# Kernel optimization log

Measured on AMD Instinct MI355X. Metric: run time of the kernel, lower is better.

## Reference

```python
import jax, jax.numpy as jnp
import numpy as np

N, IN_RAW, H, E, UNROLLS = 1024, 10, 96, 16384, 2

def _p(key, shape):
    return jax.random.normal(key, shape, dtype=jnp.float32) * 0.05

def setup_inputs() -> dict:
    key = jax.random.key(0)
    ks = jax.random.split(key, 24)
    x = jax.random.normal(ks[0], (N, IN_RAW), dtype=jnp.float32)
    edge_index = jax.random.randint(ks[1], (2, E), 0, N, dtype=jnp.int64)
    adj = jax.random.randint(ks[2], (N, N), 0, 2, dtype=jnp.int32)
    return {
        'x': x, 'edge_index': edge_index, 'adj': adj,
        # init_layer
        'W_init': _p(ks[3], (H, IN_RAW - 1)), 'b_init': _p(ks[4], (H,)),
        # GatedGraphConv (num_layers=1): weight [H,H], GRUCell params
        'W_ggc': _p(ks[5], (H, H)),
        'W_ih': _p(ks[6], (3 * H, H)), 'W_hh': _p(ks[7], (3 * H, H)),
        'b_ih': _p(ks[8], (3 * H,)), 'b_hh': _p(ks[9], (3 * H,)),
        # edge_attention: Linear(2H->H), Linear(H->1)
        'Wa1': _p(ks[10], (H, 2 * H)), 'ba1': _p(ks[11], (H,)),
        'Wa2': _p(ks[12], (1, H)), 'ba2': _p(ks[13], (1,)),
        # out MLP
        'Wo1': _p(ks[14], (H, H)), 'bo1': _p(ks[15], (H,)),
        'Wo2': _p(ks[16], (H, H)), 'bo2': _p(ks[17], (H,)),
        # heads
        'Wp1': _p(ks[18], (1, H)), 'bp1': _p(ks[19], (1,)),
        'Wp2': _p(ks[20], (1, H)), 'bp2': _p(ks[21], (1,)),
    }

def _leaky(v):
    return jnp.where(v >= 0, v, 0.01 * v)  # LeakyReLU default slope

def _ggnn_forward(x, edge_index, adj,
                  W_init, b_init, W_ggc, W_ih, W_hh, b_ih, b_hh,
                  Wa1, ba1, Wa2, ba2, Wo1, bo1, Wo2, bo2,
                  Wp1, bp1, Wp2, bp2):
    src, tgt = edge_index[0], edge_index[1]
    x = x[:, :-1]                                   # data.x[:, :-1]
    x = _leaky(x @ W_init.T + b_init)               # [N,H]
    adj_mask = (adj == 1)
    for _ in range(UNROLLS):
        # GatedGraphConv, 1 layer, aggr='mean'
        m = x @ W_ggc                               # [N,H]
        s = jax.ops.segment_sum(m[src], tgt, num_segments=N)
        cnt = jax.ops.segment_sum(jnp.ones((E,), x.dtype), tgt, num_segments=N)
        agg = s / jnp.maximum(cnt, 1.0)[:, None]    # mean, 0 for isolated nodes
        # GRUCell(agg, x)
        gi = agg @ W_ih.T + b_ih
        gh = x @ W_hh.T + b_hh
        ir, iz, inn = jnp.split(gi, 3, axis=1)
        hr, hz, hn = jnp.split(gh, 3, axis=1)
        r = jax.nn.sigmoid(ir + hr)
        z = jax.nn.sigmoid(iz + hz)
        n = jnp.tanh(inn + r * hn)
        x = (1.0 - z) * n + z * x
        # edge attention: concat(x_i, x_j) -> Linear(2H->H) decomposed into
        # two [H,H] halves so the NxNx2H concat tensor is never materialized.
        hi = x @ Wa1[:, :H].T                       # acts on t1 (row i)
        hj = x @ Wa1[:, H:].T                       # acts on t2 (row j)
        h = jax.nn.sigmoid(hi[:, None, :] + hj[None, :, :] + ba1)  # [N,N,H]
        coeffs = jax.nn.sigmoid(h @ Wa2[0] + ba2[0])               # [N,N]
        coeffs = jnp.where(adj_mask, coeffs, 0.0)
        x = coeffs @ x
    x = _leaky(x @ Wo1.T + bo1)
    x = _leaky(x @ Wo2.T + bo2)
    out1 = jax.nn.sigmoid(x @ Wp1.T + bp1)
    out2 = jax.nn.sigmoid(x @ Wp2.T + bp2)
    return out1, out2

def reference(x, edge_index, adj,
              W_init, b_init, W_ggc, W_ih, W_hh, b_ih, b_hh,
              Wa1, ba1, Wa2, ba2, Wo1, bo1, Wo2, bo2,
              Wp1, bp1, Wp2, bp2):
    return _ggnn_forward(x, edge_index, adj,
                         W_init, b_init, W_ggc, W_ih, W_hh, b_ih, b_hh,
                         Wa1, ba1, Wa2, ba2, Wo1, bo1, Wo2, bo2,
                         Wp1, bp1, Wp2, bp2)
```

## Files before the change

kernel.cpp:

```cpp
#include <hip/hip_runtime.h>

#define Nn 1024
#define Hh 96
#define Ee 16384
#define IN_K 9
#define IN_STRIDE 10
#define NH (Nn * Hh)
#define XS 128
#define SLOTS 64

__device__ __forceinline__ float sigf(float v) {
    return __builtin_amdgcn_rcpf(1.0f + __expf(-v));
}
__device__ __forceinline__ float tanhfast(float v) {
    float e = __expf(2.0f * v);
    return (e - 1.0f) * __builtin_amdgcn_rcpf(e + 1.0f);
}
__device__ __forceinline__ float leakyf(float v) {
    return v >= 0.0f ? v : 0.01f * v;
}

__global__ __launch_bounds__(1024) void setup_kernel(
    const float* __restrict__ W_hh, const float* __restrict__ Wa1,
    const float* __restrict__ Wo1, const float* __restrict__ Wo2,
    const float* __restrict__ W_ggc, const float* __restrict__ W_ih,
    const float* __restrict__ x_in, const float* __restrict__ W_init,
    const float* __restrict__ b_init, const int* __restrict__ ei,
    float* __restrict__ Wt_hh, float* __restrict__ Wt_a1i,
    float* __restrict__ Wt_a1j, float* __restrict__ Wt_o1,
    float* __restrict__ Wt_o2, float* __restrict__ Wf,
    float* __restrict__ xA, int* __restrict__ deg, int* __restrict__ bucket)
{
    int tid = threadIdx.x;
    int blk = blockIdx.x;
    int gt = blk * 1024 + tid;
    if (gt < 64512) {
        int idx = gt;
        if (idx < 27648) {
            int k = idx / 288, c = idx % 288;
            Wt_hh[idx] = W_hh[c * 96 + k];
        } else if ((idx -= 27648) < 9216) {
            int k = idx / 96, h2 = idx % 96;
            Wt_a1i[idx] = Wa1[h2 * 192 + k];
        } else if ((idx -= 9216) < 9216) {
            int k = idx / 96, h2 = idx % 96;
            Wt_a1j[idx] = Wa1[h2 * 192 + 96 + k];
        } else if ((idx -= 9216) < 9216) {
            int k = idx / 96, j = idx % 96;
            Wt_o1[idx] = Wo1[j * 96 + k];
        } else {
            idx -= 9216;
            int k = idx / 96, j = idx % 96;
            Wt_o2[idx] = Wo2[j * 96 + k];
        }
    }
    if (gt < 27648) {
        int k = gt / 288, c = gt % 288;
        const float* g = W_ggc + k * 96;
        const float* w = W_ih + c * 96;
        float acc = 0.0f;
        for (int j = 0; j < 96; ++j) acc += g[j] * w[j];
        Wf[gt] = acc;
    }
    if (gt < NH) {
        int n = gt / Hh, j = gt - n * Hh;
        const float* xr = x_in + n * IN_STRIDE;
        const float* wr = W_init + j * IN_K;
        float acc = b_init[j];
#pragma unroll
        for (int k = 0; k < IN_K; ++k) acc += xr[k] * wr[k];
        xA[n * XS + j] = leakyf(acc);
    }
    if (tid >= 960) {
        int e = blk * 64 + (tid - 960);
        int src = ei[e];
        int tgt = ei[Ee + e];
        int slot = atomicAdd(&deg[tgt], 1);
        if (slot < SLOTS) bucket[tgt * SLOTS + slot] = src;
    }
}

struct GShm {
    float Pg[2][4][Hh];
    float Pm[4][Hh];
    float Xr[4][Hh];
    float Xo[4][Hh];
    float gd[6][4][Hh];
    float redp[2][4][4][Hh];
};

__global__ __launch_bounds__(768) void gru_kernel(
    const float* __restrict__ xin, const int* __restrict__ deg,
    const int* __restrict__ bucket,
    const float* __restrict__ Wf, const float* __restrict__ Wt_hh,
    const float* __restrict__ b_ih, const float* __restrict__ b_hh,
    const float* __restrict__ Wt_a1i, const float* __restrict__ Wt_a1j,
    const float* __restrict__ ba1,
    float* __restrict__ xout, float* __restrict__ Ei, float* __restrict__ EjT)
{
    __shared__ GShm sh;
    int tid = threadIdx.x;
    int i0 = blockIdx.x * 4;

    {
        int h = tid % Hh;
        int rr = (tid / Hh) & 3;
        int s2 = tid / 384;
        int n = i0 + rr;
        int d = deg[n];
        int dc = d < SLOTS ? d : SLOTS;
        const int* bk = bucket + n * SLOTS;
        float acc = 0.0f;
        for (int s = s2; s < dc; s += 2)
            acc += xin[bk[s] * XS + h];
        sh.Pg[s2][rr][h] = acc;
        if (s2 == 0) sh.Xr[rr][h] = xin[n * XS + h];
    }
    __syncthreads();
    if (tid < 384) {
        int h = tid % Hh, rr = tid / Hh;
        float inv = __builtin_amdgcn_rcpf(fmaxf((float)deg[i0 + rr], 1.0f));
        sh.Pm[rr][h] = (sh.Pg[0][rr][h] + sh.Pg[1][rr][h]) * inv;
    }
    __syncthreads();

    if (tid < 576) {
        int h = tid % Hh;
        int g = tid / Hh;
        bool ipath = g < 3;
        int gc = ipath ? g : g - 3;
        const float* W = (ipath ? Wf : Wt_hh) + gc * 96 + h;
        const float (*src)[Hh] = ipath ? sh.Pm : sh.Xr;
        float a0 = 0.f, a1 = 0.f, a2 = 0.f, a3 = 0.f;
#pragma unroll 8
        for (int k = 0; k < 96; ++k) {
            float w = W[k * 288];
            a0 += src[0][k] * w;
            a1 += src[1][k] * w;
            a2 += src[2][k] * w;
            a3 += src[3][k] * w;
        }
        sh.gd[g][0][h] = a0;
        sh.gd[g][1][h] = a1;
        sh.gd[g][2][h] = a2;
        sh.gd[g][3][h] = a3;
    }
    __syncthreads();

    if (tid < 384) {
        int h = tid % Hh, rr = tid / Hh;
        float gir = b_ih[h]        + sh.gd[0][rr][h];
        float giz = b_ih[96 + h]   + sh.gd[1][rr][h];
        float gin = b_ih[192 + h]  + sh.gd[2][rr][h];
        float ghr = b_hh[h]        + sh.gd[3][rr][h];
        float ghz = b_hh[96 + h]   + sh.gd[4][rr][h];
        float ghn = b_hh[192 + h]  + sh.gd[5][rr][h];
        float r_  = sigf(gir + ghr);
        float z   = sigf(giz + ghz);
        float nn2 = tanhfast(gin + r_ * ghn);
        float xo  = (1.0f - z) * nn2 + z * sh.Xr[rr][h];
        xout[(i0 + rr) * XS + h] = xo;
        sh.Xo[rr][h] = xo;
    }
    __syncthreads();

    {
        int h = tid % Hh;
        int q = (tid / Hh) & 3;
        int w = tid / 384;
        const float* Wp = (w ? Wt_a1j : Wt_a1i) + h;
        float a0 = 0.f, a1 = 0.f, a2 = 0.f, a3 = 0.f;
        int k0 = q * 24;
#pragma unroll 4
        for (int k = k0; k < k0 + 24; ++k) {
            float wv = Wp[k * 96];
            a0 += sh.Xo[0][k] * wv;
            a1 += sh.Xo[1][k] * wv;
            a2 += sh.Xo[2][k] * wv;
            a3 += sh.Xo[3][k] * wv;
        }
        sh.redp[w][q][0][h] = a0;
        sh.redp[w][q][1][h] = a1;
        sh.redp[w][q][2][h] = a2;
        sh.redp[w][q][3][h] = a3;
    }
    __syncthreads();

    {
        int h = tid % Hh;
        int rr = (tid / Hh) & 3;
        int w = tid / 384;
        int n = i0 + rr;
        float s = sh.redp[w][0][rr][h] + sh.redp[w][1][rr][h]
                + sh.redp[w][2][rr][h] + sh.redp[w][3][rr][h];
        if (w == 0) Ei[n * Hh + h]  = __expf(-(s + ba1[h]));
        else        EjT[h * Nn + n] = __expf(-s);
    }
}

__global__ __launch_bounds__(1024) void attn_kernel_u0(
    const float* __restrict__ Ei, const float* __restrict__ EjT,
    const float* __restrict__ Wa2, const float* __restrict__ ba2,
    const int* __restrict__ adj, const float* __restrict__ xB,
    float* __restrict__ xOut)
{
    __shared__ float sm[7168];
    __shared__ float eis[4 * Hh];
    __shared__ float wa2s[Hh];
    int tid = threadIdx.x;
    int i0 = blockIdx.x * 4;
    if (tid < 4 * Hh) eis[tid] = Ei[i0 * Hh + tid];
    if (tid >= 512 && tid < 512 + Hh) wa2s[tid - 512] = Wa2[tid - 512];
    {
        int j = tid;
        int m0 = adj[(i0 + 0) * Nn + j];
        int m1 = adj[(i0 + 1) * Nn + j];
        int m2 = adj[(i0 + 2) * Nn + j];
        int m3 = adj[(i0 + 3) * Nn + j];
        __syncthreads();
        float s0 = 0.f, s1 = 0.f, s2 = 0.f, s3 = 0.f;
#pragma unroll 8
        for (int k = 0; k < Hh; ++k) {
            float e = EjT[k * Nn + j];
            float wk = wa2s[k];
            s0 += __builtin_amdgcn_rcpf(fmaf(eis[k], e, 1.0f)) * wk;
            s1 += __builtin_amdgcn_rcpf(fmaf(eis[96 + k], e, 1.0f)) * wk;
            s2 += __builtin_amdgcn_rcpf(fmaf(eis[192 + k], e, 1.0f)) * wk;
            s3 += __builtin_amdgcn_rcpf(fmaf(eis[288 + k], e, 1.0f)) * wk;
        }
        float b2 = ba2[0];
        sm[0 * Nn + j] = (m0 == 1) ? sigf(s0 + b2) : 0.0f;
        sm[1 * Nn + j] = (m1 == 1) ? sigf(s1 + b2) : 0.0f;
        sm[2 * Nn + j] = (m2 == 1) ? sigf(s2 + b2) : 0.0f;
        sm[3 * Nn + j] = (m3 == 1) ? sigf(s3 + b2) : 0.0f;
    }
    __syncthreads();
    {
        int q = tid >> 7;
        int h = tid & 127;
        if (h < Hh) {
            int jb = q * 128;
            const float* xc = xB + jb * XS + h;
            const float* c0 = sm + 0 * Nn + jb;
            const float* c1 = sm + 1 * Nn + jb;
            const float* c2 = sm + 2 * Nn + jb;
            const float* c3 = sm + 3 * Nn + jb;
            float a0 = 0.f, a1 = 0.f, a2 = 0.f, a3 = 0.f;
#pragma unroll 4
            for (int j = 0; j < 128; ++j) {
                float xv = xc[j * XS];
                a0 += c0[j] * xv;
                a1 += c1[j] * xv;
                a2 += c2[j] * xv;
                a3 += c3[j] * xv;
            }
            sm[4096 + ((q * 4 + 0) * Hh) + h] = a0;
            sm[4096 + ((q * 4 + 1) * Hh) + h] = a1;
            sm[4096 + ((q * 4 + 2) * Hh) + h] = a2;
            sm[4096 + ((q * 4 + 3) * Hh) + h] = a3;
        }
    }
    __syncthreads();
    if (tid < 4 * Hh) {
        int r = tid / Hh, h = tid - r * Hh;
        float v = 0.f;
#pragma unroll
        for (int q = 0; q < 8; ++q)
            v += sm[4096 + ((q * 4 + r) * Hh) + h];
        xOut[(i0 + r) * XS + h] = v;
    }
}

__global__ __launch_bounds__(1024) void attn_kernel_u1(
    const float* __restrict__ Ei, const float* __restrict__ EjT,
    const float* __restrict__ Wa2, const float* __restrict__ ba2,
    const int* __restrict__ adj, const float* __restrict__ xB,
    const float* __restrict__ Wt_o1, const float* __restrict__ bo1,
    const float* __restrict__ Wt_o2, const float* __restrict__ bo2,
    const float* __restrict__ Wp1, const float* __restrict__ bp1,
    const float* __restrict__ Wp2, const float* __restrict__ bp2,
    float* __restrict__ out)
{
    __shared__ float sm[7168];
    __shared__ float eis[4 * Hh];
    __shared__ float wa2s[Hh];
    __shared__ float hd[3][4][Hh];
    int tid = threadIdx.x;
    int i0 = blockIdx.x * 4;
    if (tid < 4 * Hh) eis[tid] = Ei[i0 * Hh + tid];
    if (tid >= 512 && tid < 512 + Hh) wa2s[tid - 512] = Wa2[tid - 512];
    {
        int j = tid;
        int m0 = adj[(i0 + 0) * Nn + j];
        int m1 = adj[(i0 + 1) * Nn + j];
        int m2 = adj[(i0 + 2) * Nn + j];
        int m3 = adj[(i0 + 3) * Nn + j];
        __syncthreads();
        float s0 = 0.f, s1 = 0.f, s2 = 0.f, s3 = 0.f;
#pragma unroll 8
        for (int k = 0; k < Hh; ++k) {
            float e = EjT[k * Nn + j];
            float wk = wa2s[k];
            s0 += __builtin_amdgcn_rcpf(fmaf(eis[k], e, 1.0f)) * wk;
            s1 += __builtin_amdgcn_rcpf(fmaf(eis[96 + k], e, 1.0f)) * wk;
            s2 += __builtin_amdgcn_rcpf(fmaf(eis[192 + k], e, 1.0f)) * wk;
            s3 += __builtin_amdgcn_rcpf(fmaf(eis[288 + k], e, 1.0f)) * wk;
        }
        float b2 = ba2[0];
        sm[0 * Nn + j] = (m0 == 1) ? sigf(s0 + b2) : 0.0f;
        sm[1 * Nn + j] = (m1 == 1) ? sigf(s1 + b2) : 0.0f;
        sm[2 * Nn + j] = (m2 == 1) ? sigf(s2 + b2) : 0.0f;
        sm[3 * Nn + j] = (m3 == 1) ? sigf(s3 + b2) : 0.0f;
    }
    __syncthreads();
    {
        int q = tid >> 7;
        int h = tid & 127;
        if (h < Hh) {
            int jb = q * 128;
            const float* xc = xB + jb * XS + h;
            const float* c0 = sm + 0 * Nn + jb;
            const float* c1 = sm + 1 * Nn + jb;
            const float* c2 = sm + 2 * Nn + jb;
            const float* c3 = sm + 3 * Nn + jb;
            float a0 = 0.f, a1 = 0.f, a2 = 0.f, a3 = 0.f;
#pragma unroll 4
            for (int j = 0; j < 128; ++j) {
                float xv = xc[j * XS];
                a0 += c0[j] * xv;
                a1 += c1[j] * xv;
                a2 += c2[j] * xv;
                a3 += c3[j] * xv;
            }
            sm[4096 + ((q * 4 + 0) * Hh) + h] = a0;
            sm[4096 + ((q * 4 + 1) * Hh) + h] = a1;
            sm[4096 + ((q * 4 + 2) * Hh) + h] = a2;
            sm[4096 + ((q * 4 + 3) * Hh) + h] = a3;
        }
    }
    __syncthreads();
    if (tid < 4 * Hh) {
        int r = tid / Hh, h = tid - r * Hh;
        float v = 0.f;
#pragma unroll
        for (int q = 0; q < 8; ++q)
            v += sm[4096 + ((q * 4 + r) * Hh) + h];
        hd[0][r][h] = v;
    }
    __syncthreads();
    if (tid < 4 * Hh) {
        int r = tid / Hh, h = tid - r * Hh;
        const float* w = Wt_o1 + h;
        const float* xr = hd[0][r];
        float acc = bo1[h];
        for (int k = 0; k < Hh; ++k) acc += xr[k] * w[k * 96];
        hd[1][r][h] = leakyf(acc);
    }
    __syncthreads();
    if (tid < 4 * Hh) {
        int r = tid / Hh, h = tid - r * Hh;
        const float* w = Wt_o2 + h;
        const float* xr = hd[1][r];
        float acc = bo2[h];
        for (int k = 0; k < Hh; ++k) acc += xr[k] * w[k * 96];
        hd[2][r][h] = leakyf(acc);
    }
    __syncthreads();
    if (tid < 8) {
        int r = tid >> 1, which = tid & 1;
        const float* wp = which ? Wp2 : Wp1;
        const float* xr = hd[2][r];
        float acc = 0.f;
        for (int k = 0; k < Hh; ++k) acc += xr[k] * wp[k];
        float b = which ? bp2[0] : bp1[0];
        out[which * Nn + i0 + r] = sigf(acc + b);
    }
}

extern "C" void kernel_launch(void* const* d_in, const int* in_sizes, int n_in,
                              void* d_out, int out_size, void* d_ws, size_t ws_size,
                              hipStream_t stream)
{
    const float* x_in   = (const float*)d_in[0];
    const int*   ei     = (const int*)d_in[1];
    const int*   adj    = (const int*)d_in[2];
    const float* W_init = (const float*)d_in[3];
    const float* b_init = (const float*)d_in[4];
    const float* W_ggc  = (const float*)d_in[5];
    const float* W_ih   = (const float*)d_in[6];
    const float* W_hh   = (const float*)d_in[7];
    const float* b_ih   = (const float*)d_in[8];
    const float* b_hh   = (const float*)d_in[9];
    const float* Wa1    = (const float*)d_in[10];
    const float* ba1    = (const float*)d_in[11];
    const float* Wa2    = (const float*)d_in[12];
    const float* ba2    = (const float*)d_in[13];
    const float* Wo1    = (const float*)d_in[14];
    const float* bo1    = (const float*)d_in[15];
    const float* Wo2    = (const float*)d_in[16];
    const float* bo2    = (const float*)d_in[17];
    const float* Wp1    = (const float*)d_in[18];
    const float* bp1    = (const float*)d_in[19];
    const float* Wp2    = (const float*)d_in[20];
    const float* bp2    = (const float*)d_in[21];
    float* out = (float*)d_out;

    float* ws     = (float*)d_ws;
    float* xA     = ws;
    float* xB     = xA + Nn * XS;
    float* xC     = xB + Nn * XS;
    float* Ei     = xC + Nn * XS;
    float* EjT    = Ei + NH;
    float* Wt_hh  = EjT + NH;
    float* Wf     = Wt_hh + 27648;
    float* Wt_a1i = Wf + 27648;
    float* Wt_a1j = Wt_a1i + 9216;
    float* Wt_o1  = Wt_a1j + 9216;
    float* Wt_o2  = Wt_o1 + 9216;
    int*   deg    = (int*)(Wt_o2 + 9216);
    int*   bucket = deg + Nn;

    hipMemsetAsync(deg, 0, Nn * sizeof(int), stream);

    setup_kernel<<<256, 1024, 0, stream>>>(
        W_hh, Wa1, Wo1, Wo2, W_ggc, W_ih, x_in, W_init, b_init, ei,
        Wt_hh, Wt_a1i, Wt_a1j, Wt_o1, Wt_o2, Wf, xA, deg, bucket);

    gru_kernel<<<256, 768, 0, stream>>>(
        xA, deg, bucket, Wf, Wt_hh, b_ih, b_hh, Wt_a1i, Wt_a1j, ba1,
        xB, Ei, EjT);
    attn_kernel_u0<<<256, 1024, 0, stream>>>(
        Ei, EjT, Wa2, ba2, adj, xB, xC);

    gru_kernel<<<256, 768, 0, stream>>>(
        xC, deg, bucket, Wf, Wt_hh, b_ih, b_hh, Wt_a1i, Wt_a1j, ba1,
        xB, Ei, EjT);
    attn_kernel_u1<<<256, 1024, 0, stream>>>(
        Ei, EjT, Wa2, ba2, adj, xB,
        Wt_o1, bo1, Wt_o2, bo2, Wp1, bp1, Wp2, bp2, out);
}
```

Baseline: 196.1 us.

## Build per-block neighbor lists in shared memory instead of global buckets

Drops the global degree/bucket construction (memset plus atomics in setup_kernel). Each GRU block now scans the full target-index array and gathers, in LDS, the sources for its four nodes using shared atomics. This removes a memset launch and shrinks setup_kernel to 96 blocks. In exchange every GRU block re-reads all 16K target indices on each unroll, and the mean aggregation now loops serially over neighbors instead of split across two thread halves.

```diff
diff --git a/kernel.cpp b/kernel.cpp
--- a/kernel.cpp
+++ b/kernel.cpp
@@ -25,15 +25,13 @@
     const float* __restrict__ Wo1, const float* __restrict__ Wo2,
     const float* __restrict__ W_ggc, const float* __restrict__ W_ih,
     const float* __restrict__ x_in, const float* __restrict__ W_init,
-    const float* __restrict__ b_init, const int* __restrict__ ei,
+    const float* __restrict__ b_init,
     float* __restrict__ Wt_hh, float* __restrict__ Wt_a1i,
     float* __restrict__ Wt_a1j, float* __restrict__ Wt_o1,
     float* __restrict__ Wt_o2, float* __restrict__ Wf,
-    float* __restrict__ xA, int* __restrict__ deg, int* __restrict__ bucket)
+    float* __restrict__ xA)
 {
-    int tid = threadIdx.x;
-    int blk = blockIdx.x;
-    int gt = blk * 1024 + tid;
+    int gt = blockIdx.x * 1024 + threadIdx.x;
     if (gt < 64512) {
         int idx = gt;
         if (idx < 27648) {
@@ -71,17 +69,11 @@
         for (int k = 0; k < IN_K; ++k) acc += xr[k] * wr[k];
         xA[n * XS + j] = leakyf(acc);
     }
-    if (tid >= 960) {
-        int e = blk * 64 + (tid - 960);
-        int src = ei[e];
-        int tgt = ei[Ee + e];
-        int slot = atomicAdd(&deg[tgt], 1);
-        if (slot < SLOTS) bucket[tgt * SLOTS + slot] = src;
-    }
 }
 
 struct GShm {
-    float Pg[2][4][Hh];
+    int   cnt[4];
+    int   lst[4][SLOTS];
     float Pm[4][Hh];
     float Xr[4][Hh];
     float Xo[4][Hh];
@@ -90,8 +82,7 @@
 };
 
 __global__ __launch_bounds__(768) void gru_kernel(
-    const float* __restrict__ xin, const int* __restrict__ deg,
-    const int* __restrict__ bucket,
+    const float* __restrict__ xin, const int* __restrict__ ei,
     const float* __restrict__ Wf, const float* __restrict__ Wt_hh,
     const float* __restrict__ b_ih, const float* __restrict__ b_hh,
     const float* __restrict__ Wt_a1i, const float* __restrict__ Wt_a1j,
@@ -102,25 +93,28 @@
     int tid = threadIdx.x;
     int i0 = blockIdx.x * 4;
 
-    {
-        int h = tid % Hh;
-        int rr = (tid / Hh) & 3;
-        int s2 = tid / 384;
-        int n = i0 + rr;
-        int d = deg[n];
-        int dc = d < SLOTS ? d : SLOTS;
-        const int* bk = bucket + n * SLOTS;
-        float acc = 0.0f;
-        for (int s = s2; s < dc; s += 2)
-            acc += xin[bk[s] * XS + h];
-        sh.Pg[s2][rr][h] = acc;
-        if (s2 == 0) sh.Xr[rr][h] = xin[n * XS + h];
-    }
-    __syncthreads();
+    if (tid < 4) sh.cnt[tid] = 0;
+    __syncthreads();
+    for (int e = tid; e < Ee; e += 768) {
+        int tgt = ei[Ee + e];
+        unsigned r = (unsigned)(tgt - i0);
+        if (r < 4u) {
+            int slot = atomicAdd(&sh.cnt[r], 1);
+            if (slot < SLOTS) sh.lst[r][slot] = ei[e];
+        }
+    }
+    __syncthreads();
+
     if (tid < 384) {
         int h = tid % Hh, rr = tid / Hh;
-        float inv = __builtin_amdgcn_rcpf(fmaxf((float)deg[i0 + rr], 1.0f));
-        sh.Pm[rr][h] = (sh.Pg[0][rr][h] + sh.Pg[1][rr][h]) * inv;
+        int d = sh.cnt[rr];
+        int dc = d < SLOTS ? d : SLOTS;
+        float acc = 0.0f;
+        for (int s = 0; s < dc; ++s)
+            acc += xin[sh.lst[rr][s] * XS + h];
+        float inv = __builtin_amdgcn_rcpf(fmaxf((float)d, 1.0f));
+        sh.Pm[rr][h] = acc * inv;
+        sh.Xr[rr][h] = xin[(i0 + rr) * XS + h];
     }
     __syncthreads();
 
@@ -417,23 +411,19 @@
     float* Wt_a1j = Wt_a1i + 9216;
     float* Wt_o1  = Wt_a1j + 9216;
     float* Wt_o2  = Wt_o1 + 9216;
-    int*   deg    = (int*)(Wt_o2 + 9216);
-    int*   bucket = deg + Nn;
-
-    hipMemsetAsync(deg, 0, Nn * sizeof(int), stream);
-
-    setup_kernel<<<256, 1024, 0, stream>>>(
-        W_hh, Wa1, Wo1, Wo2, W_ggc, W_ih, x_in, W_init, b_init, ei,
-        Wt_hh, Wt_a1i, Wt_a1j, Wt_o1, Wt_o2, Wf, xA, deg, bucket);
+
+    setup_kernel<<<96, 1024, 0, stream>>>(
+        W_hh, Wa1, Wo1, Wo2, W_ggc, W_ih, x_in, W_init, b_init,
+        Wt_hh, Wt_a1i, Wt_a1j, Wt_o1, Wt_o2, Wf, xA);
 
     gru_kernel<<<256, 768, 0, stream>>>(
-        xA, deg, bucket, Wf, Wt_hh, b_ih, b_hh, Wt_a1i, Wt_a1j, ba1,
+        xA, ei, Wf, Wt_hh, b_ih, b_hh, Wt_a1i, Wt_a1j, ba1,
         xB, Ei, EjT);
     attn_kernel_u0<<<256, 1024, 0, stream>>>(
         Ei, EjT, Wa2, ba2, adj, xB, xC);
 
     gru_kernel<<<256, 768, 0, stream>>>(
-        xC, deg, bucket, Wf, Wt_hh, b_ih, b_hh, Wt_a1i, Wt_a1j, ba1,
+        xC, ei, Wf, Wt_hh, b_ih, b_hh, Wt_a1i, Wt_a1j, ba1,
         xB, Ei, EjT);
     attn_kernel_u1<<<256, 1024, 0, stream>>>(
         Ei, EjT, Wa2, ba2, adj, xB,
```

Result: no change. 198.2 us (+1.1%).
